# Optimization experiments

Measured on AMD Instinct MI355X. Metric: run time of the kernel, lower is better.

The kernel has to match this reference:

```python
import jax, jax.numpy as jnp
import numpy as np

N = 50000      # num nodes
E = 1_600_000  # num edges
D = 64         # in_dim == hidden_dim
H = 4          # heads
C = 16         # head_dim = hidden_dim // heads
NEG = 0.2      # leaky_relu negative slope (PyG GATConv default)


def setup_inputs() -> dict:
    key = jax.random.key(0)
    ks = jax.random.split(key, 20)
    f = lambda k, s: (jax.random.normal(k, s, jnp.float32) * 0.1)
    return dict(
        node_features=jax.random.normal(ks[0], (N, D), jnp.float32),
        edge_index=jax.random.randint(ks[1], (2, E), 0, N, dtype=jnp.int32),
        edge_type=jax.random.randint(ks[2], (E,), 0, 5, dtype=jnp.int32),
        edge_attr=jax.random.normal(ks[3], (E, 1), jnp.float32),
        # GAT layer 1 (PyG GATConv: lin has no bias, att_* are [H,C], final bias [H*C])
        W1=f(ks[4], (D, H * C)), att_src1=f(ks[5], (H, C)), att_dst1=f(ks[6], (H, C)),
        We1=f(ks[7], (1, H * C)), att_e1=f(ks[8], (H, C)), b1=jnp.zeros((H * C,), jnp.float32),
        # GAT layer 2
        W2=f(ks[9], (D, H * C)), att_src2=f(ks[10], (H, C)), att_dst2=f(ks[11], (H, C)),
        We2=f(ks[12], (1, H * C)), att_e2=f(ks[13], (H, C)), b2=jnp.zeros((H * C,), jnp.float32),
        # LayerNorms
        g1=jnp.ones((D,), jnp.float32), beta1=jnp.zeros((D,), jnp.float32),
        g2=jnp.ones((D,), jnp.float32), beta2=jnp.zeros((D,), jnp.float32),
        # output head
        Wout=f(ks[14], (D, 1)), bout=jnp.zeros((1,), jnp.float32),
    )


def _layernorm(x, g, b, eps=1e-5):
    mu = x.mean(-1, keepdims=True)
    v = ((x - mu) ** 2).mean(-1, keepdims=True)
    return (x - mu) * jax.lax.rsqrt(v + eps) * g + b


def _seg_softmax(alpha, dst, n):
    # numerically stable segment softmax over incoming edges of each dst node
    m = jax.ops.segment_max(alpha, dst, num_segments=n)
    m = jnp.where(jnp.isfinite(m), m, 0.0)
    ex = jnp.exp(alpha - m[dst])
    den = jax.ops.segment_sum(ex, dst, num_segments=n)
    return ex / (den[dst] + 1e-16)


def _gatconv(x, src, dst, eattr, W, a_s, a_d, We, a_e, b, n):
    xs = (x @ W).reshape(n, H, C)                       # [N,H,C]
    a_src = jnp.einsum('nhc,hc->nh', xs, a_s)           # [N,H]
    a_dst = jnp.einsum('nhc,hc->nh', xs, a_d)           # [N,H]
    ee = (eattr @ We).reshape(-1, H, C)                 # [E',H,C]
    a_edge = jnp.einsum('ehc,hc->eh', ee, a_e)          # [E',H]
    alpha = a_src[src] + a_dst[dst] + a_edge            # [E',H]
    alpha = jax.nn.leaky_relu(alpha, NEG)
    alpha = _seg_softmax(alpha, dst, n)                 # [E',H]
    msg = xs[src] * alpha[..., None]                    # [E',H,C] gather-weighted messages
    out = jax.ops.segment_sum(msg, dst, num_segments=n) # scatter-aggregate
    return out.reshape(n, H * C) + b


def reference(node_features, edge_index, edge_type, edge_attr,
              W1, att_src1, att_dst1, We1, att_e1, b1,
              W2, att_src2, att_dst2, We2, att_e2, b2,
              g1, beta1, g2, beta2, Wout, bout):
    src, dst = edge_index[0], edge_index[1]
    # PyG add_self_loops(fill_value='mean'): self-loop edge_attr = mean of edge_attr over incoming edges
    cnt = jax.ops.segment_sum(jnp.ones((E,), jnp.float32), dst, num_segments=N)
    loop_attr = jax.ops.segment_sum(edge_attr, dst, num_segments=N) / jnp.maximum(cnt, 1.0)[:, None]
    loops = jnp.arange(N, dtype=src.dtype)
    src2 = jnp.concatenate([src, loops])
    dst2 = jnp.concatenate([dst, loops])
    ea = jnp.concatenate([edge_attr, loop_attr], axis=0)

    residual = node_features  # in_dim == hidden_dim -> no res_proj
    h = _gatconv(node_features, src2, dst2, ea, W1, att_src1, att_dst1, We1, att_e1, b1, N)
    h = jax.nn.elu(_layernorm(h + residual, g1, beta1))
    residual = h
    h = _gatconv(h, src2, dst2, ea, W2, att_src2, att_dst2, We2, att_e2, b2, N)
    h = jax.nn.elu(_layernorm(h + residual, g2, beta2))
    return h @ Wout + bout
```

## Files before the change

### kernel.cpp

```cpp
#include <hip/hip_runtime.h>
#include <hip/hip_bf16.h>
#include <cfloat>

#define NN 50000
#define NE 1600000
#define NEG 0.2f
#define NBKT 196
#define BNODE 256
#define P1_TILE 2048
#define P1_BLOCKS 782
#define GEMM_BLOCKS 391
#define BCAP 8704
#define SLOTS 96
#define L2E 1.4426950408889634f
#define SMEM_BYTES 10880

typedef __attribute__((ext_vector_type(8))) short bf8_t;
typedef __attribute__((ext_vector_type(4))) float f4_t;

__device__ __forceinline__ float bf16bits_to_f(unsigned v) {
  return __uint_as_float(v << 16);
}
__device__ __forceinline__ unsigned f_to_bf16bits(float f) {
  unsigned u = __float_as_uint(f);
  return (u + 0x7fffu + ((u >> 16) & 1u)) >> 16;
}

__device__ __forceinline__ bf8_t pack8(const float* p) {
  bf8_t r;
#pragma unroll
  for (int i = 0; i < 8; ++i) r[i] = (short)f_to_bf16bits(p[i]);
  return r;
}

__device__ void bin_body(char* smem, int blk, const int* __restrict__ src,
                         const int* __restrict__ dst,
                         const float* __restrict__ ea, int* __restrict__ gcnt,
                         int2* __restrict__ gbuf) {
  int* lcnt = (int*)smem;
  int* lcur = lcnt + NBKT;
  int t = threadIdx.x;
  if (t < NBKT) lcnt[t] = 0;
  __syncthreads();
  int e0 = blk * P1_TILE + t * 8;
  int bb[8], vx[8], vy[8];
  if (e0 + 8 <= NE) {
    int4 d0 = *(const int4*)(dst + e0), d1 = *(const int4*)(dst + e0 + 4);
    int4 s0 = *(const int4*)(src + e0), s1 = *(const int4*)(src + e0 + 4);
    int4 a0 = *(const int4*)((const int*)ea + e0);
    int4 a1 = *(const int4*)((const int*)ea + e0 + 4);
    int dd[8] = {d0.x, d0.y, d0.z, d0.w, d1.x, d1.y, d1.z, d1.w};
    int ss[8] = {s0.x, s0.y, s0.z, s0.w, s1.x, s1.y, s1.z, s1.w};
    int aa[8] = {a0.x, a0.y, a0.z, a0.w, a1.x, a1.y, a1.z, a1.w};
#pragma unroll
    for (int k = 0; k < 8; ++k) {
      bb[k] = dd[k] >> 8;
      vx[k] = ((dd[k] & 255) << 16) | ss[k];
      vy[k] = aa[k];
      atomicAdd(&lcnt[bb[k]], 1);
    }
  } else {
#pragma unroll
    for (int k = 0; k < 8; ++k) {
      int e = e0 + k;
      if (e < NE) {
        int d = dst[e];
        bb[k] = d >> 8;
        vx[k] = ((d & 255) << 16) | src[e];
        vy[k] = __float_as_int(ea[e]);
        atomicAdd(&lcnt[bb[k]], 1);
      } else {
        bb[k] = -1;
      }
    }
  }
  __syncthreads();
  if (t < NBKT) lcur[t] = atomicAdd(&gcnt[t], lcnt[t]);
  __syncthreads();
#pragma unroll
  for (int k = 0; k < 8; ++k) {
    if (bb[k] >= 0) {
      int pos = atomicAdd(&lcur[bb[k]], 1);
      if (pos < BCAP) gbuf[(size_t)bb[k] * BCAP + pos] = make_int2(vx[k], vy[k]);
    }
  }
}

template <bool FP32IN>
__device__ void gemm_body(char* smem, int blk, const void* __restrict__ xin,
                          const float* __restrict__ W,
                          const float* __restrict__ att_s,
                          const float* __restrict__ att_d,
                          unsigned short* __restrict__ xsb,
                          float* __restrict__ a_src,
                          float* __restrict__ a_dst) {
  unsigned short(*Wt)[68] = (unsigned short(*)[68])smem;
  int t = threadIdx.x;
  for (int i = t; i < 4096; i += 256) {
    int k = i >> 6, n = i & 63;
    Wt[n][k] = (unsigned short)f_to_bf16bits(W[i]);
  }
  __syncthreads();
  {
    int k = t & 63, h = t >> 6;
    float ps = 0.f, pd = 0.f;
#pragma unroll
    for (int c = 0; c < 16; ++c) {
      float w = bf16bits_to_f(Wt[h * 16 + c][k]);
      ps = fmaf(w, att_s[h * 16 + c], ps);
      pd = fmaf(w, att_d[h * 16 + c], pd);
    }
    Wt[64 + h][k] = (unsigned short)f_to_bf16bits(ps * L2E);
    Wt[68 + h][k] = (unsigned short)f_to_bf16bits(pd * L2E);
    Wt[72 + h][k] = 0;
    Wt[76 + h][k] = 0;
  }
  __syncthreads();
  int lane = t & 63, wave = t >> 6;
  int quad = lane >> 4, n16 = lane & 15;

  bf8_t bfrag[5][2];
#pragma unroll
  for (int nt = 0; nt < 5; ++nt)
#pragma unroll
    for (int kk = 0; kk < 2; ++kk)
      bfrag[nt][kk] = *(const bf8_t*)&Wt[nt * 16 + n16][kk * 32 + quad * 8];

#pragma unroll
  for (int set = 0; set < 2; ++set) {
    int r0 = blk * 128 + set * 64 + wave * 16;
    int rowA = r0 + n16; if (rowA > NN - 1) rowA = NN - 1;
    bf8_t af0, af1;
    if (FP32IN) {
      const float* xr = (const float*)xin + (size_t)rowA * 64 + quad * 8;
      af0 = pack8(xr);
      af1 = pack8(xr + 32);
    } else {
      const bf8_t* xrow =
          (const bf8_t*)((const unsigned short*)xin + (size_t)rowA * 64);
      af0 = xrow[quad];
      af1 = xrow[4 + quad];
    }
#pragma unroll
    for (int nt = 0; nt < 5; ++nt) {
      f4_t acc = {0.f, 0.f, 0.f, 0.f};
      acc = __builtin_amdgcn_mfma_f32_16x16x32_bf16(af0, bfrag[nt][0], acc, 0, 0, 0);
      acc = __builtin_amdgcn_mfma_f32_16x16x32_bf16(af1, bfrag[nt][1], acc, 0, 0, 0);
      if (nt < 4) {
#pragma unroll
        for (int reg = 0; reg < 4; ++reg) {
          int row = r0 + quad * 4 + reg;
          if (row < NN)
            xsb[(size_t)row * 64 + nt * 16 + n16] =
                (unsigned short)f_to_bf16bits(acc[reg]);
        }
      } else {
#pragma unroll
        for (int reg = 0; reg < 4; ++reg) {
          int row = r0 + quad * 4 + reg;
          if (row < NN && n16 < 8) {
            if (n16 < 4) a_src[row * 4 + n16] = acc[reg];
            else a_dst[row * 4 + (n16 - 4)] = acc[reg];
          }
        }
      }
    }
  }
}

__global__ __launch_bounds__(256) void front_kernel(
    const int* __restrict__ src, const int* __restrict__ dst,
    const float* __restrict__ ea, int* __restrict__ gcnt,
    int2* __restrict__ gbuf, const float* __restrict__ x,
    const float* __restrict__ W1, const float* __restrict__ as1,
    const float* __restrict__ ad1, unsigned short* __restrict__ xsb,
    float* __restrict__ a_src, float* __restrict__ a_dst) {
  __shared__ __align__(16) char smem[SMEM_BYTES];
  if (blockIdx.x < P1_BLOCKS) {
    bin_body(smem, blockIdx.x, src, dst, ea, gcnt, gbuf);
  } else {
    gemm_body<true>(smem, blockIdx.x - P1_BLOCKS, x, W1, as1, ad1, xsb, a_src,
                    a_dst);
  }
}

__global__ __launch_bounds__(256) void gemm2_kernel(
    const unsigned short* __restrict__ xin, const float* __restrict__ W,
    const float* __restrict__ att_s, const float* __restrict__ att_d,
    unsigned short* __restrict__ xsb, float* __restrict__ a_src,
    float* __restrict__ a_dst) {
  __shared__ __align__(16) char smem[SMEM_BYTES];
  gemm_body<false>(smem, blockIdx.x, xin, W, att_s, att_d, xsb, a_src, a_dst);
}

__global__ __launch_bounds__(1024) void build_kernel(
    const int* __restrict__ gcnt, const int2* __restrict__ gbuf,
    int* __restrict__ cnt, unsigned* __restrict__ csr) {
  __shared__ int lc[BNODE];
  int t = threadIdx.x;
  int b = blockIdx.x;
  if (t < BNODE) lc[t] = 0;
  __syncthreads();
  int len = gcnt[b]; if (len > BCAP) len = BCAP;
  const int2* buf = gbuf + (size_t)b * BCAP;
  for (int i = t; i < len; i += 1024) {
    int2 v = buf[i];
    int dl = (v.x >> 16) & 255;
    int s = v.x & 0xffff;
    int pos = atomicAdd(&lc[dl], 1);
    if (pos < SLOTS) {
      unsigned eb = ((unsigned)v.y) & 0xffff0000u;
      csr[(size_t)(b * BNODE + dl) * SLOTS + pos] = eb | (unsigned)s;
    }
  }
  __syncthreads();
  if (t < BNODE) {
    int n = b * BNODE + t;
    if (n < NN) cnt[n] = min(lc[t], SLOTS);
  }
}

template <bool HEAD>
__global__ __launch_bounds__(256) void aggregate_kernel(
    const int* __restrict__ cnt, const unsigned* __restrict__ csr,
    const unsigned short* __restrict__ xsb, const float* __restrict__ a_src,
    const float* __restrict__ a_dst, const float* __restrict__ We,
    const float* __restrict__ att_e, const float* __restrict__ bias,
    const void* __restrict__ resv, const float* __restrict__ g,
    const float* __restrict__ beta, const float* __restrict__ Wout,
    const float* __restrict__ bout, float* __restrict__ out,
    unsigned short* __restrict__ out_b) {
  __shared__ __align__(16) uint2 rec[4][64][4];
  int t = threadIdx.x;
  int lane = t & 63, wave = t >> 6;
  int half = lane >> 5;
  int d2 = lane & 31;
  int hb = d2 >> 3;
  int n = blockIdx.x * 8 + wave * 2 + half;

  float sp = We[lane] * att_e[lane];
#pragma unroll
  for (int off = 8; off; off >>= 1) sp += __shfl_xor(sp, off, 16);
  sp *= L2E;
  float s0 = __shfl(sp, 0, 64), s1 = __shfl(sp, 16, 64);
  float s2 = __shfl(sp, 32, 64), s3 = __shfl(sp, 48, 64);

  const float4 adv = *(const float4*)(a_dst + (size_t)n * 4);

  int dn = cnt[n];
  int mdn = max(dn, __shfl_xor(dn, 32, 64));
  float accx = 0.f, accy = 0.f, den = 0.f, easum = 0.f;
  const uint2* rpb = &rec[wave][half * 32][hb];
  const char* xd = (const char*)xsb + d2 * 4;

  for (int base = 0; base < mdn; base += 32) {
    int c = mdn - base; if (c > 32) c = 32;
    int el = base + d2;
    unsigned ce = (el < dn) ? csr[(size_t)n * SLOTS + el] : 0u;
    float ea = __uint_as_float(ce & 0xffff0000u);
    easum += ea;
    unsigned soff = (ce & 0xffffu) * 128u;
    float ex0 = 0.f, ex1 = 0.f, ex2 = 0.f, ex3 = 0.f;
    if (el < dn) {
      const float4 av = *(const float4*)(a_src + (size_t)(ce & 0xffffu) * 4);
      float a0 = av.x + fmaf(ea, s0, adv.x); a0 = fmaxf(a0, NEG * a0);
      float a1 = av.y + fmaf(ea, s1, adv.y); a1 = fmaxf(a1, NEG * a1);
      float a2 = av.z + fmaf(ea, s2, adv.z); a2 = fmaxf(a2, NEG * a2);
      float a3 = av.w + fmaf(ea, s3, adv.w); a3 = fmaxf(a3, NEG * a3);
      ex0 = exp2f(a0); ex1 = exp2f(a1); ex2 = exp2f(a2); ex3 = exp2f(a3);
    }
    uint4* wp = (uint4*)&rec[wave][lane][0];
    wp[0] = make_uint4(soff, __float_as_uint(ex0), soff, __float_as_uint(ex1));
    wp[1] = make_uint4(soff, __float_as_uint(ex2), soff, __float_as_uint(ex3));
    int c8 = (c + 7) & ~7;
    for (int j = 0; j < c8; j += 8) {
      uint2 v0 = rpb[(j + 0) * 4];
      uint2 v1 = rpb[(j + 1) * 4];
      uint2 v2 = rpb[(j + 2) * 4];
      uint2 v3 = rpb[(j + 3) * 4];
      uint2 v4 = rpb[(j + 4) * 4];
      uint2 v5 = rpb[(j + 5) * 4];
      uint2 v6 = rpb[(j + 6) * 4];
      uint2 v7 = rpb[(j + 7) * 4];
      unsigned u0 = *(const unsigned*)(xd + v0.x);
      unsigned u1 = *(const unsigned*)(xd + v1.x);
      unsigned u2 = *(const unsigned*)(xd + v2.x);
      unsigned u3 = *(const unsigned*)(xd + v3.x);
      unsigned u4 = *(const unsigned*)(xd + v4.x);
      unsigned u5 = *(const unsigned*)(xd + v5.x);
      unsigned u6 = *(const unsigned*)(xd + v6.x);
      unsigned u7 = *(const unsigned*)(xd + v7.x);
      float e0f = __uint_as_float(v0.y), e1f = __uint_as_float(v1.y);
      float e2f = __uint_as_float(v2.y), e3f = __uint_as_float(v3.y);
      float e4f = __uint_as_float(v4.y), e5f = __uint_as_float(v5.y);
      float e6f = __uint_as_float(v6.y), e7f = __uint_as_float(v7.y);
      den += ((e0f + e1f) + (e2f + e3f)) + ((e4f + e5f) + (e6f + e7f));
      accx = fmaf(e0f, __uint_as_float(u0 << 16), accx);
      accy = fmaf(e0f, __uint_as_float(u0 & 0xffff0000u), accy);
      accx = fmaf(e1f, __uint_as_float(u1 << 16), accx);
      accy = fmaf(e1f, __uint_as_float(u1 & 0xffff0000u), accy);
      accx = fmaf(e2f, __uint_as_float(u2 << 16), accx);
      accy = fmaf(e2f, __uint_as_float(u2 & 0xffff0000u), accy);
      accx = fmaf(e3f, __uint_as_float(u3 << 16), accx);
      accy = fmaf(e3f, __uint_as_float(u3 & 0xffff0000u), accy);
      accx = fmaf(e4f, __uint_as_float(u4 << 16), accx);
      accy = fmaf(e4f, __uint_as_float(u4 & 0xffff0000u), accy);
      accx = fmaf(e5f, __uint_as_float(u5 << 16), accx);
      accy = fmaf(e5f, __uint_as_float(u5 & 0xffff0000u), accy);
      accx = fmaf(e6f, __uint_as_float(u6 << 16), accx);
      accy = fmaf(e6f, __uint_as_float(u6 & 0xffff0000u), accy);
      accx = fmaf(e7f, __uint_as_float(u7 << 16), accx);
      accy = fmaf(e7f, __uint_as_float(u7 & 0xffff0000u), accy);
    }
  }

#pragma unroll
  for (int off = 16; off; off >>= 1) easum += __shfl_xor(easum, off, 32);

  float loop_ea = easum / fmaxf((float)dn, 1.0f);
  float as_h = a_src[(size_t)n * 4 + hb];
  float adn = (hb == 0) ? adv.x : (hb == 1) ? adv.y : (hb == 2) ? adv.z : adv.w;
  float sph = (hb == 0) ? s0 : (hb == 1) ? s1 : (hb == 2) ? s2 : s3;
  float a_self = as_h + fmaf(loop_ea, sph, adn);
  a_self = fmaxf(a_self, NEG * a_self);
  float ex_self = exp2f(a_self);
  den += ex_self;
  unsigned un = *(const unsigned*)((const char*)xsb + (size_t)n * 128 + d2 * 4);
  accx = fmaf(ex_self, __uint_as_float(un << 16), accx);
  accy = fmaf(ex_self, __uint_as_float(un & 0xffff0000u), accy);

  float rden = 1.f / (den + 1e-16f);
  const float2 bi = *(const float2*)(bias + d2 * 2);
  float2 rsd;
  if (HEAD) {
    unsigned ur =
        *(const unsigned*)((const unsigned short*)resv + (size_t)n * 64 + d2 * 2);
    rsd.x = bf16bits_to_f(ur & 0xffffu);
    rsd.y = __uint_as_float(ur & 0xffff0000u);
  } else {
    rsd = *(const float2*)((const float*)resv + (size_t)n * 64 + d2 * 2);
  }
  float vx = accx * rden + bi.x + rsd.x;
  float vy = accy * rden + bi.y + rsd.y;
  float s = vx + vy;
#pragma unroll
  for (int off = 16; off; off >>= 1) s += __shfl_xor(s, off, 32);
  float mu = s * (1.0f / 64.0f);
  float dx = vx - mu, dy = vy - mu;
  float var = dx * dx + dy * dy;
#pragma unroll
  for (int off = 16; off; off >>= 1) var += __shfl_xor(var, off, 32);
  var *= (1.0f / 64.0f);
  float rstd = rsqrtf(var + 1e-5f);
  const float2 gg = *(const float2*)(g + d2 * 2);
  const float2 bb = *(const float2*)(beta + d2 * 2);
  float yx = dx * rstd * gg.x + bb.x;
  float yy = dy * rstd * gg.y + bb.y;
  yx = yx > 0.f ? yx : expm1f(yx);
  yy = yy > 0.f ? yy : expm1f(yy);
  if (HEAD) {
    const float2 wv = *(const float2*)(Wout + d2 * 2);
    float p = yx * wv.x + yy * wv.y;
#pragma unroll
    for (int off = 16; off; off >>= 1) p += __shfl_xor(p, off, 32);
    if (d2 == 0) out[n] = p + bout[0];
  } else {
    unsigned ob = f_to_bf16bits(yx) | (f_to_bf16bits(yy) << 16);
    *(unsigned*)(out_b + (size_t)n * 64 + d2 * 2) = ob;
  }
}

extern "C" void kernel_launch(void* const* d_in, const int* in_sizes, int n_in,
                              void* d_out, int out_size, void* d_ws,
                              size_t ws_size, hipStream_t stream) {
  const float* node_features = (const float*)d_in[0];
  const int* edge_index = (const int*)d_in[1];
  const int* src = edge_index;
  const int* dst = edge_index + NE;
  const float* edge_attr = (const float*)d_in[3];
  const float* W1 = (const float*)d_in[4];
  const float* att_src1 = (const float*)d_in[5];
  const float* att_dst1 = (const float*)d_in[6];
  const float* We1 = (const float*)d_in[7];
  const float* att_e1 = (const float*)d_in[8];
  const float* b1 = (const float*)d_in[9];
  const float* W2 = (const float*)d_in[10];
  const float* att_src2 = (const float*)d_in[11];
  const float* att_dst2 = (const float*)d_in[12];
  const float* We2 = (const float*)d_in[13];
  const float* att_e2 = (const float*)d_in[14];
  const float* b2 = (const float*)d_in[15];
  const float* g1 = (const float*)d_in[16];
  const float* beta1 = (const float*)d_in[17];
  const float* g2 = (const float*)d_in[18];
  const float* beta2 = (const float*)d_in[19];
  const float* Wout = (const float*)d_in[20];
  const float* bout = (const float*)d_in[21];
  float* out = (float*)d_out;

  char* ws = (char*)d_ws;
  size_t o = 0;
  auto alloc = [&](size_t bytes) {
    void* p = ws + o;
    o += (bytes + 255) & ~(size_t)255;
    return p;
  };
  int* gcnt = (int*)alloc((size_t)NBKT * 4);
  int2* gbuf = (int2*)alloc((size_t)NBKT * BCAP * 8);
  int* cnt = (int*)alloc((size_t)NN * 4);
  unsigned* csr = (unsigned*)alloc((size_t)NN * SLOTS * 4);
  unsigned short* xsb = (unsigned short*)alloc((size_t)NN * 64 * 2);
  unsigned short* h1b = (unsigned short*)alloc((size_t)NN * 64 * 2);
  float* a_srcb = (float*)alloc((size_t)NN * 4 * 4);
  float* a_dstb = (float*)alloc((size_t)NN * 4 * 4);

  hipMemsetAsync(gcnt, 0, (size_t)NBKT * 4, stream);

  front_kernel<<<P1_BLOCKS + GEMM_BLOCKS, 256, 0, stream>>>(
      src, dst, edge_attr, gcnt, gbuf, node_features, W1, att_src1, att_dst1,
      xsb, a_srcb, a_dstb);
  build_kernel<<<NBKT, 1024, 0, stream>>>(gcnt, gbuf, cnt, csr);

  aggregate_kernel<false><<<NN / 8, 256, 0, stream>>>(
      cnt, csr, xsb, a_srcb, a_dstb, We1, att_e1, b1, node_features, g1, beta1,
      nullptr, nullptr, nullptr, h1b);

  gemm2_kernel<<<GEMM_BLOCKS, 256, 0, stream>>>(h1b, W2, att_src2, att_dst2,
                                                xsb, a_srcb, a_dstb);
  aggregate_kernel<true><<<NN / 8, 256, 0, stream>>>(
      cnt, csr, xsb, a_srcb, a_dstb, We2, att_e2, b2, h1b, g2, beta2, Wout,
      bout, out, nullptr);
}
```

Measured before the change: 236.0 us.

## Bin edges into per-block fixed-capacity slots instead of global atomic buckets

Each binning block now writes its edges into a private fixed-size slot (SCAP=40) per bucket and stores a per-block count, which removes the global atomicAdd on bucket counters, the extra shared-memory counting pass and the memset. The build kernel then walks per-source-block slots, one thread per source block, to fill the CSR. The cost is a larger, sparser staging buffer. The build kernel also loses parallelism, since only 782 of its 1024 threads have work and each walks its slot serially. Edges beyond 40 per block-bucket are dropped, though the expected load is about 10.

```diff
diff --git a/kernel.cpp b/kernel.cpp
--- a/kernel.cpp
+++ b/kernel.cpp
@@ -10,7 +10,7 @@
 #define P1_TILE 2048
 #define P1_BLOCKS 782
 #define GEMM_BLOCKS 391
-#define BCAP 8704
+#define SCAP 40
 #define SLOTS 96
 #define L2E 1.4426950408889634f
 #define SMEM_BYTES 10880
@@ -35,12 +35,11 @@
 
 __device__ void bin_body(char* smem, int blk, const int* __restrict__ src,
                          const int* __restrict__ dst,
-                         const float* __restrict__ ea, int* __restrict__ gcnt,
+                         const float* __restrict__ ea, int* __restrict__ scnt,
                          int2* __restrict__ gbuf) {
-  int* lcnt = (int*)smem;
-  int* lcur = lcnt + NBKT;
+  int* lcur = (int*)smem;
   int t = threadIdx.x;
-  if (t < NBKT) lcnt[t] = 0;
+  if (t < NBKT) lcur[t] = 0;
   __syncthreads();
   int e0 = blk * P1_TILE + t * 8;
   int bb[8], vx[8], vy[8];
@@ -57,7 +56,6 @@
       bb[k] = dd[k] >> 8;
       vx[k] = ((dd[k] & 255) << 16) | ss[k];
       vy[k] = aa[k];
-      atomicAdd(&lcnt[bb[k]], 1);
     }
   } else {
 #pragma unroll
@@ -68,22 +66,22 @@
         bb[k] = d >> 8;
         vx[k] = ((d & 255) << 16) | src[e];
         vy[k] = __float_as_int(ea[e]);
-        atomicAdd(&lcnt[bb[k]], 1);
       } else {
         bb[k] = -1;
       }
     }
   }
-  __syncthreads();
-  if (t < NBKT) lcur[t] = atomicAdd(&gcnt[t], lcnt[t]);
-  __syncthreads();
 #pragma unroll
   for (int k = 0; k < 8; ++k) {
     if (bb[k] >= 0) {
       int pos = atomicAdd(&lcur[bb[k]], 1);
-      if (pos < BCAP) gbuf[(size_t)bb[k] * BCAP + pos] = make_int2(vx[k], vy[k]);
-    }
-  }
+      if (pos < SCAP)
+        gbuf[((size_t)bb[k] * P1_BLOCKS + blk) * SCAP + pos] =
+            make_int2(vx[k], vy[k]);
+    }
+  }
+  __syncthreads();
+  if (t < NBKT) scnt[blk * NBKT + t] = min(lcur[t], SCAP);
 }
 
 template <bool FP32IN>
@@ -170,14 +168,14 @@
 
 __global__ __launch_bounds__(256) void front_kernel(
     const int* __restrict__ src, const int* __restrict__ dst,
-    const float* __restrict__ ea, int* __restrict__ gcnt,
+    const float* __restrict__ ea, int* __restrict__ scnt,
     int2* __restrict__ gbuf, const float* __restrict__ x,
     const float* __restrict__ W1, const float* __restrict__ as1,
     const float* __restrict__ ad1, unsigned short* __restrict__ xsb,
     float* __restrict__ a_src, float* __restrict__ a_dst) {
   __shared__ __align__(16) char smem[SMEM_BYTES];
   if (blockIdx.x < P1_BLOCKS) {
-    bin_body(smem, blockIdx.x, src, dst, ea, gcnt, gbuf);
+    bin_body(smem, blockIdx.x, src, dst, ea, scnt, gbuf);
   } else {
     gemm_body<true>(smem, blockIdx.x - P1_BLOCKS, x, W1, as1, ad1, xsb, a_src,
                     a_dst);
@@ -194,23 +192,25 @@
 }
 
 __global__ __launch_bounds__(1024) void build_kernel(
-    const int* __restrict__ gcnt, const int2* __restrict__ gbuf,
+    const int* __restrict__ scnt, const int2* __restrict__ gbuf,
     int* __restrict__ cnt, unsigned* __restrict__ csr) {
   __shared__ int lc[BNODE];
   int t = threadIdx.x;
   int b = blockIdx.x;
   if (t < BNODE) lc[t] = 0;
   __syncthreads();
-  int len = gcnt[b]; if (len > BCAP) len = BCAP;
-  const int2* buf = gbuf + (size_t)b * BCAP;
-  for (int i = t; i < len; i += 1024) {
-    int2 v = buf[i];
-    int dl = (v.x >> 16) & 255;
-    int s = v.x & 0xffff;
-    int pos = atomicAdd(&lc[dl], 1);
-    if (pos < SLOTS) {
-      unsigned eb = ((unsigned)v.y) & 0xffff0000u;
-      csr[(size_t)(b * BNODE + dl) * SLOTS + pos] = eb | (unsigned)s;
+  for (int s = t; s < P1_BLOCKS; s += 1024) {
+    int c = scnt[s * NBKT + b];
+    const int2* p = gbuf + ((size_t)b * P1_BLOCKS + s) * SCAP;
+    for (int i = 0; i < c; ++i) {
+      int2 v = p[i];
+      int dl = (v.x >> 16) & 255;
+      int pos = atomicAdd(&lc[dl], 1);
+      if (pos < SLOTS) {
+        unsigned eb = ((unsigned)v.y) & 0xffff0000u;
+        csr[(size_t)(b * BNODE + dl) * SLOTS + pos] =
+            eb | (unsigned)(v.x & 0xffff);
+      }
     }
   }
   __syncthreads();
@@ -405,8 +405,8 @@
     o += (bytes + 255) & ~(size_t)255;
     return p;
   };
-  int* gcnt = (int*)alloc((size_t)NBKT * 4);
-  int2* gbuf = (int2*)alloc((size_t)NBKT * BCAP * 8);
+  int* scnt = (int*)alloc((size_t)P1_BLOCKS * NBKT * 4);
+  int2* gbuf = (int2*)alloc((size_t)NBKT * P1_BLOCKS * SCAP * 8);
   int* cnt = (int*)alloc((size_t)NN * 4);
   unsigned* csr = (unsigned*)alloc((size_t)NN * SLOTS * 4);
   unsigned short* xsb = (unsigned short*)alloc((size_t)NN * 64 * 2);
@@ -414,12 +414,10 @@
   float* a_srcb = (float*)alloc((size_t)NN * 4 * 4);
   float* a_dstb = (float*)alloc((size_t)NN * 4 * 4);
 
-  hipMemsetAsync(gcnt, 0, (size_t)NBKT * 4, stream);
-
   front_kernel<<<P1_BLOCKS + GEMM_BLOCKS, 256, 0, stream>>>(
-      src, dst, edge_attr, gcnt, gbuf, node_features, W1, att_src1, att_dst1,
+      src, dst, edge_attr, scnt, gbuf, node_features, W1, att_src1, att_dst1,
       xsb, a_srcb, a_dstb);
-  build_kernel<<<NBKT, 1024, 0, stream>>>(gcnt, gbuf, cnt, csr);
+  build_kernel<<<NBKT, 1024, 0, stream>>>(scnt, gbuf, cnt, csr);
 
   aggregate_kernel<false><<<NN / 8, 256, 0, stream>>>(
       cnt, csr, xsb, a_srcb, a_dstb, We1, att_e1, b1, node_features, g1, beta1,
```

Result: no change. 235.2 us (median of 2 runs) (-0.4%).
